# Performance work log

Hardware: AMD Instinct MI355X
Metric: run time of the kernel (lower is better)

The kernel has to match this reference:

```python
import jax, jax.numpy as jnp
import numpy as np

B, S, E, H, T = 32, 4096, 256, 256, 64  # bsz, seq_len, enc_dim, lstm_hid, turns/sample


def setup_inputs() -> dict:
    key = jax.random.key(0)
    k1, k2, k3, k4, k5, k6, k7 = jax.random.split(key, 7)
    encoder_output = jax.random.normal(k1, (B, S, E), dtype=jnp.float32)
    # equal-length turn structure: even partition of [0, S) into T non-empty segments
    ends = (jnp.arange(1, T + 1, dtype=jnp.int32) * S) // T - 1  # [T], strictly increasing
    his_turn_end_ids = jnp.broadcast_to(ends, (B, T))
    s = 1.0 / np.sqrt(H)
    W_ih = jax.random.uniform(k2, (4 * H, E), minval=-s, maxval=s, dtype=jnp.float32)
    W_hh = jax.random.uniform(k3, (4 * H, H), minval=-s, maxval=s, dtype=jnp.float32)
    b_ih = jax.random.uniform(k4, (4 * H,), minval=-s, maxval=s, dtype=jnp.float32)
    b_hh = jax.random.uniform(k5, (4 * H,), minval=-s, maxval=s, dtype=jnp.float32)
    sf = 1.0 / np.sqrt(H + E)
    fc_w = jax.random.uniform(k6, (1, H + E), minval=-sf, maxval=sf, dtype=jnp.float32)
    fc_b = jax.random.uniform(k7, (1,), minval=-sf, maxval=sf, dtype=jnp.float32)
    return {"encoder_output": encoder_output, "his_turn_end_ids": his_turn_end_ids,
            "W_ih": W_ih, "W_hh": W_hh, "b_ih": b_ih, "b_hh": b_hh,
            "fc_w": fc_w, "fc_b": fc_b}


def _lstm_cell(x, h, c, W_ih, W_hh, b):
    g = x @ W_ih.T + h @ W_hh.T + b          # [N, 4H], torch gate order i,f,g,o
    i, f, gg, o = jnp.split(g, 4, axis=-1)
    c = jax.nn.sigmoid(f) * c + jax.nn.sigmoid(i) * jnp.tanh(gg)
    h = jax.nn.sigmoid(o) * jnp.tanh(c)
    return h, c


def reference(encoder_output, his_turn_end_ids, W_ih, W_hh, b_ih, b_hh, fc_w, fc_b):
    Bc, Sc, Ec = encoder_output.shape
    Tc = his_turn_end_ids.shape[1]
    ends = his_turn_end_ids.astype(jnp.int32)
    starts = jnp.concatenate([jnp.zeros((Bc, 1), jnp.int32), ends[:, :-1] + 1], axis=1)
    # segment mean via exclusive prefix sum: sum[s:e+1] = csum[e+1] - csum[s]
    csum = jnp.concatenate([jnp.zeros((Bc, 1, Ec), encoder_output.dtype),
                            jnp.cumsum(encoder_output, axis=1)], axis=1)  # [B, S+1, E]
    seg_sum = (jnp.take_along_axis(csum, (ends + 1)[..., None], axis=1)
               - jnp.take_along_axis(csum, starts[..., None], axis=1))   # [B, T, E]
    lens = (ends - starts + 1).astype(encoder_output.dtype)
    states = seg_sum / lens[..., None]                                   # his_turn_states

    # length-2 LSTM over (state_j, state_{j+1}) for each anchor j in [0, T-3]
    J = Tc - 2
    x1 = states[:, :J].reshape(-1, Ec)       # [B*J, E]
    x2 = states[:, 1:J + 1].reshape(-1, Ec)
    b = b_ih + b_hh
    h0 = jnp.zeros((x1.shape[0], W_hh.shape[1]), states.dtype)
    h1, c1 = _lstm_cell(x1, h0, h0, W_ih, W_hh, b)
    h2, _ = _lstm_cell(x2, h1, c1, W_ih, W_hh, b)
    src_last = h2.reshape(Bc, J, -1)         # [B, J, H]

    # logit(i,j,k) = fc([src_last[i,j]; states[i, j+2+k]]) for k < T-2-j
    Wh, We = fc_w[0, :src_last.shape[-1]], fc_w[0, src_last.shape[-1]:]
    a = src_last @ Wh                        # [B, J]
    t = states @ We                          # [B, T]
    jdx = jnp.arange(J)
    kdx = jnp.arange(J)
    tgt_idx = jdx[:, None] + 2 + kdx[None, :]        # [J, J]
    valid = tgt_idx < Tc
    tgt_idx = jnp.clip(tgt_idx, 0, Tc - 1)
    logits = a[:, :, None] + t[:, tgt_idx] + fc_b[0]  # [B, J, J]
    neg_inf = jnp.asarray(-1e30, logits.dtype)
    masked = jnp.where(valid[None], logits, neg_inf)
    # CE with target class 0 (first candidate, the true next turn)
    loss = jax.nn.logsumexp(masked, axis=-1) - logits[..., 0]  # [B, J]
    return jnp.mean(loss)


if __name__ == "__main__":
    out = reference(**setup_inputs())
    print(out)
```

## Files before the change

kernel.cpp:

```cpp
#include <hip/hip_runtime.h>
#include <math.h>

#define B 32
#define S 4096
#define E 256
#define H 256
#define T 64
#define J (T - 2)

__global__ __launch_bounds__(256) void row_dot_kernel(
    const float* __restrict__ enc,
    const float* __restrict__ We,
    float* __restrict__ d) {
    const int gid  = blockIdx.x * blockDim.x + threadIdx.x;
    const int row  = gid >> 6;
    const int lane = threadIdx.x & 63;

    const float4* rowp = reinterpret_cast<const float4*>(enc + (size_t)row * E);
    const float4  v = rowp[lane];
    const float4  w = reinterpret_cast<const float4*>(We)[lane];
    float p = v.x * w.x + v.y * w.y + v.z * w.z + v.w * w.w;

#pragma unroll
    for (int off = 32; off >= 1; off >>= 1)
        p += __shfl_xor(p, off, 64);

    if (lane == 0) d[row] = p;
}

__global__ __launch_bounds__(64) void seg_loss_kernel(
    const float* __restrict__ d,
    const int* __restrict__ ends,
    float* __restrict__ loss_b) {
    const int b   = blockIdx.x;
    const int tau = threadIdx.x;

    __shared__ float tt[T];

    const int e  = ends[b * T + tau];
    const int st = (tau == 0) ? 0 : (ends[b * T + tau - 1] + 1);
    float s = 0.0f;
    for (int i = st; i <= e; ++i) s += d[b * S + i];
    tt[tau] = s / (float)(e - st + 1);
    __syncthreads();

    float lj = 0.0f;
    if (tau < J) {
        float M = -1e30f;
        for (int m = tau + 2; m < T; ++m) M = fmaxf(M, tt[m]);
        float acc = 0.0f;
        for (int m = tau + 2; m < T; ++m) acc += expf(tt[m] - M);
        lj = logf(acc) + M - tt[tau + 2];
    }

#pragma unroll
    for (int off = 32; off >= 1; off >>= 1)
        lj += __shfl_xor(lj, off, 64);

    if (tau == 0) loss_b[b] = lj;
}

__global__ __launch_bounds__(64) void final_kernel(
    const float* __restrict__ loss_b,
    float* __restrict__ out) {
    const int lane = threadIdx.x;
    float v = (lane < B) ? loss_b[lane] : 0.0f;
#pragma unroll
    for (int off = 32; off >= 1; off >>= 1)
        v += __shfl_xor(v, off, 64);
    if (lane == 0) out[0] = v / (float)(B * J);
}

extern "C" void kernel_launch(void* const* d_in, const int* in_sizes, int n_in,
                              void* d_out, int out_size, void* d_ws, size_t ws_size,
                              hipStream_t stream) {
    const float* enc  = (const float*)d_in[0];
    const int*   ends = (const int*)d_in[1];
    const float* fc_w = (const float*)d_in[6];
    const float* We   = fc_w + H;

    float* d      = (float*)d_ws;
    float* loss_b = d + (size_t)B * S;
    float* out    = (float*)d_out;

    row_dot_kernel<<<(B * S) / 4, 256, 0, stream>>>(enc, We, d);
    seg_loss_kernel<<<B, 64, 0, stream>>>(d, ends, loss_b);
    final_kernel<<<1, 64, 0, stream>>>(loss_b, out);
}
```

Measured before the change: 43.11 us.

## Fuse segment mean into dot kernel and merge loss and final reduction

Each block now handles one (batch, turn) segment: four wavefronts accumulate encoder rows into a per-segment sum vector, combine it through LDS, and take a single dot product with We. This replaces the per-row dot products, the intermediate per-row buffer, and the serial per-thread segment sum. The per-batch loss kernel and the final reduction are merged into one single-block kernel, dropping one launch. Per-block work now depends on segment length, so load balance could suffer with uneven turn lengths.

```diff
diff --git a/kernel.cpp b/kernel.cpp
--- a/kernel.cpp
+++ b/kernel.cpp
@@ -8,67 +8,82 @@
 #define T 64
 #define J (T - 2)
 
-__global__ __launch_bounds__(256) void row_dot_kernel(
+__global__ __launch_bounds__(256) void seg_dot_kernel(
     const float* __restrict__ enc,
+    const int* __restrict__ ends,
     const float* __restrict__ We,
-    float* __restrict__ d) {
-    const int gid  = blockIdx.x * blockDim.x + threadIdx.x;
-    const int row  = gid >> 6;
+    float* __restrict__ t) {
+    const int g    = blockIdx.x;
+    const int tau  = g & (T - 1);
+    const int b    = g >> 6;
+    const int w    = threadIdx.x >> 6;
     const int lane = threadIdx.x & 63;
 
-    const float4* rowp = reinterpret_cast<const float4*>(enc + (size_t)row * E);
-    const float4  v = rowp[lane];
-    const float4  w = reinterpret_cast<const float4*>(We)[lane];
-    float p = v.x * w.x + v.y * w.y + v.z * w.z + v.w * w.w;
+    const int e  = ends[g];
+    const int st = (tau == 0) ? 0 : (ends[g - 1] + 1);
 
+    const float4* base = reinterpret_cast<const float4*>(enc + (size_t)b * S * E);
+    float4 acc = {0.f, 0.f, 0.f, 0.f};
+#pragma unroll 4
+    for (int r = st + w; r <= e; r += 4) {
+        float4 v = base[(size_t)r * 64 + lane];
+        acc.x += v.x; acc.y += v.y; acc.z += v.z; acc.w += v.w;
+    }
+
+    __shared__ float4 lds[256];
+    lds[threadIdx.x] = acc;
+    __syncthreads();
+
+    if (w == 0) {
+        float4 a0 = lds[lane];
+        float4 a1 = lds[64 + lane];
+        float4 a2 = lds[128 + lane];
+        float4 a3 = lds[192 + lane];
+        float4 wv = reinterpret_cast<const float4*>(We)[lane];
+        float p = (a0.x + a1.x + a2.x + a3.x) * wv.x
+                + (a0.y + a1.y + a2.y + a3.y) * wv.y
+                + (a0.z + a1.z + a2.z + a3.z) * wv.z
+                + (a0.w + a1.w + a2.w + a3.w) * wv.w;
 #pragma unroll
-    for (int off = 32; off >= 1; off >>= 1)
-        p += __shfl_xor(p, off, 64);
-
-    if (lane == 0) d[row] = p;
+        for (int off = 32; off >= 1; off >>= 1)
+            p += __shfl_xor(p, off, 64);
+        if (lane == 0) t[g] = p / (float)(e - st + 1);
+    }
 }
 
-__global__ __launch_bounds__(64) void seg_loss_kernel(
-    const float* __restrict__ d,
-    const int* __restrict__ ends,
-    float* __restrict__ loss_b) {
-    const int b   = blockIdx.x;
-    const int tau = threadIdx.x;
+__global__ __launch_bounds__(512) void loss_kernel(
+    const float* __restrict__ t,
+    float* __restrict__ out) {
+    __shared__ float tt[B * T];
+    __shared__ float partial[8];
+    const int tid = threadIdx.x;
 
-    __shared__ float tt[T];
-
-    const int e  = ends[b * T + tau];
-    const int st = (tau == 0) ? 0 : (ends[b * T + tau - 1] + 1);
-    float s = 0.0f;
-    for (int i = st; i <= e; ++i) s += d[b * S + i];
-    tt[tau] = s / (float)(e - st + 1);
+    for (int i = tid; i < B * T; i += 512) tt[i] = t[i];
     __syncthreads();
 
-    float lj = 0.0f;
-    if (tau < J) {
+    float sum = 0.f;
+    for (int item = tid; item < B * J; item += 512) {
+        const int b = item / J;
+        const int j = item - b * J;
+        const float* tb = tt + b * T;
         float M = -1e30f;
-        for (int m = tau + 2; m < T; ++m) M = fmaxf(M, tt[m]);
-        float acc = 0.0f;
-        for (int m = tau + 2; m < T; ++m) acc += expf(tt[m] - M);
-        lj = logf(acc) + M - tt[tau + 2];
+        for (int m = j + 2; m < T; ++m) M = fmaxf(M, tb[m]);
+        float acc = 0.f;
+        for (int m = j + 2; m < T; ++m) acc += __expf(tb[m] - M);
+        sum += logf(acc) + M - tb[j + 2];
     }
 
 #pragma unroll
     for (int off = 32; off >= 1; off >>= 1)
-        lj += __shfl_xor(lj, off, 64);
+        sum += __shfl_xor(sum, off, 64);
+    if ((tid & 63) == 0) partial[tid >> 6] = sum;
+    __syncthreads();
 
-    if (tau == 0) loss_b[b] = lj;
-}
-
-__global__ __launch_bounds__(64) void final_kernel(
-    const float* __restrict__ loss_b,
-    float* __restrict__ out) {
-    const int lane = threadIdx.x;
-    float v = (lane < B) ? loss_b[lane] : 0.0f;
-#pragma unroll
-    for (int off = 32; off >= 1; off >>= 1)
-        v += __shfl_xor(v, off, 64);
-    if (lane == 0) out[0] = v / (float)(B * J);
+    if (tid == 0) {
+        float tot = 0.f;
+        for (int i = 0; i < 8; ++i) tot += partial[i];
+        out[0] = tot / (float)(B * J);
+    }
 }
 
 extern "C" void kernel_launch(void* const* d_in, const int* in_sizes, int n_in,
@@ -76,14 +91,11 @@
                               hipStream_t stream) {
     const float* enc  = (const float*)d_in[0];
     const int*   ends = (const int*)d_in[1];
-    const float* fc_w = (const float*)d_in[6];
-    const float* We   = fc_w + H;
+    const float* We   = (const float*)d_in[6] + H;
 
-    float* d      = (float*)d_ws;
-    float* loss_b = d + (size_t)B * S;
-    float* out    = (float*)d_out;
+    float* t   = (float*)d_ws;
+    float* out = (float*)d_out;
 
-    row_dot_kernel<<<(B * S) / 4, 256, 0, stream>>>(enc, We, d);
-    seg_loss_kernel<<<B, 64, 0, stream>>>(d, ends, loss_b);
-    final_kernel<<<1, 64, 0, stream>>>(loss_b, out);
+    seg_dot_kernel<<<B * T, 256, 0, stream>>>(enc, ends, We, t);
+    loss_kernel<<<1, 512, 0, stream>>>(t, out);
 }
```

New measurement: 46.34 us. 1.07x slower.
